# Optimization experiments

Hardware: AMD Instinct MI355X
Metric: run time of the kernel (lower is better)

## Reference

```python
import jax, jax.numpy as jnp
from jax import lax
import numpy as np

IMG = 800
SUB = 16
FS = IMG // SUB            # 50
NA = 9                     # 3 ratios x 3 scales
PRE_NMS = 6000             # test-mode n_test_pre_nms
POST_NMS = 300             # test-mode n_test_post_nms
NMS_THRESH = 0.7
MIN_BOX = 16.0
SLOPE = 0.01               # nn.LeakyReLU default


def build_anchors():
    # Faithful to _generate_anchor: x outer loop, y inner; ctr = grid - 8;
    # anchor rows are [x1, y1, w, h]; ratio outer, scale inner.
    c = np.arange(SUB, (FS + 1) * SUB, SUB).astype(np.float32) - 8.0  # 50 centers
    cx = np.repeat(c, FS)   # x is the outer loop
    cy = np.tile(c, FS)     # y is the inner loop
    rs = np.array([0.5, 1.0, 2.0], dtype=np.float32)
    ss = np.array([8.0, 16.0, 32.0], dtype=np.float32)
    hs = (SUB * ss[None, :] * np.sqrt(rs)[:, None]).reshape(-1)        # [9]
    ws = (SUB * ss[None, :] * np.sqrt(1.0 / rs)[:, None]).reshape(-1)  # [9]
    x1 = cx[:, None] - ws[None, :] / 2.0   # [2500, 9]
    y1 = cy[:, None] - hs[None, :] / 2.0
    w = np.broadcast_to(ws[None, :], x1.shape)
    h = np.broadcast_to(hs[None, :], x1.shape)
    return np.stack([x1, y1, w, h], axis=-1).reshape(-1, 4).astype(np.float32)  # [22500, 4]


def _conv(x, w, b, pad):
    y = lax.conv_general_dilated(x, w, (1, 1), ((pad, pad), (pad, pad)),
                                 dimension_numbers=("NCHW", "OIHW", "NCHW"))
    return y + b[None, :, None, None]


def _nms_keep(boxes):
    # Greedy NMS over score-sorted boxes [P,4] = (x1,y1,x2,y2); returns keep mask.
    x1, y1, x2, y2 = boxes[:, 0], boxes[:, 1], boxes[:, 2], boxes[:, 3]
    area = (x2 - x1 + 1.0) * (y2 - y1 + 1.0)
    P = boxes.shape[0]
    idx = jnp.arange(P)

    def body(i, keep):
        xx1 = jnp.maximum(x1[i], x1)
        yy1 = jnp.maximum(y1[i], y1)
        xx2 = jnp.minimum(x2[i], x2)
        yy2 = jnp.maximum(y2[i], y2)  # faithful to source bug: np.maximum, not minimum
        w = jnp.maximum(0.0, xx2 - xx1 + 1.0)
        h = jnp.maximum(0.0, yy2 - yy1 + 1.0)
        inter = w * h
        ov = inter / (area[i] + area - inter)
        suppress = (ov > NMS_THRESH) & (idx > i) & keep[i]
        return keep & ~suppress

    return lax.fori_loop(0, P, body, jnp.ones((P,), dtype=bool))


def _forward(in_features, conv_w, conv_b, reg_w, reg_b, cls_w, cls_b):
    B = in_features.shape[0]
    feat = _conv(in_features, conv_w, conv_b, 1)
    feat = jnp.where(feat >= 0, feat, SLOPE * feat)  # LeakyReLU(0.01)
    reg = _conv(feat, reg_w, reg_b, 0).transpose(0, 2, 3, 1).reshape(B, -1, 4)
    cls = _conv(feat, cls_w, cls_b, 0).transpose(0, 2, 3, 1).reshape(B, -1, 2)
    cls = jax.nn.softmax(cls, axis=2)

    anchors = jnp.asarray(build_anchors())  # [A,4] = (x1,y1,w,h)
    # The torch loop overwrites `rois` each batch iteration and returns only the
    # last batch's proposals; compute that directly.
    pr = reg[-1]                 # [A,4]
    score = cls[-1, :, 1]        # [A]
    hi = jnp.float32(IMG - 1)
    rx1 = jnp.clip(pr[:, 0] + anchors[:, 0], 0.0, hi)
    ry1 = jnp.clip(pr[:, 1] + anchors[:, 1], 0.0, hi)
    rx2 = jnp.clip(pr[:, 0] + anchors[:, 0] + pr[:, 2] + anchors[:, 2], 0.0, hi)
    ry2 = jnp.clip(pr[:, 1] + anchors[:, 1] + pr[:, 3] + anchors[:, 3], 0.0, hi)
    w = pr[:, 2] + anchors[:, 2]  # unclipped, as in source
    h = pr[:, 3] + anchors[:, 3]
    valid = (w >= MIN_BOX) & (h >= MIN_BOX)
    s = jnp.where(valid, score, -jnp.inf)   # filtered boxes sort to the end
    order = jnp.argsort(-s)[:PRE_NMS]       # top-6000 valid by objectness
    boxes = jnp.stack([rx1, ry1, rx2, ry2], axis=1)[order]  # [PRE,4]

    keep = _nms_keep(lax.stop_gradient(boxes))
    # first POST_NMS surviving boxes, in score order
    sel = jnp.argsort(jnp.where(keep, jnp.arange(PRE_NMS), PRE_NMS))[:POST_NMS]
    kb = boxes[sel]
    # output format: x1, y1, w, h
    return jnp.stack([kb[:, 0], kb[:, 1],
                      kb[:, 2] - kb[:, 0] + 1.0,
                      kb[:, 3] - kb[:, 1] + 1.0], axis=1)


def setup_inputs() -> dict:
    key = jax.random.key(0)
    k = jax.random.split(key, 4)
    return {
        "in_features": jax.random.normal(k[0], (8, 512, FS, FS), dtype=jnp.float32),
        "conv_w": jax.random.normal(k[1], (512, 512, 3, 3), dtype=jnp.float32) * 0.02,
        "conv_b": jnp.zeros((512,), dtype=jnp.float32),
        "reg_w": jax.random.normal(k[2], (36, 512, 1, 1), dtype=jnp.float32) * 0.02,
        "reg_b": jnp.zeros((36,), dtype=jnp.float32),
        "cls_w": jax.random.normal(k[3], (18, 512, 1, 1), dtype=jnp.float32) * 0.02,
        "cls_b": jnp.zeros((18,), dtype=jnp.float32),
    }


def reference(in_features, conv_w, conv_b, reg_w, reg_b, cls_w, cls_b):
    return _forward(in_features, conv_w, conv_b, reg_w, reg_b, cls_w, cls_b)
```

## Files before the change

### kernel.cpp

```cpp
#include <hip/hip_runtime.h>


#define NPIX 2500
#define NANCH 22500
#define NKEY 22528
#define PRE 6000
#define MASKW 94
#define MW 96
#define JCHUNK 1536
#define CS 8
#define KSLOT 8
#define PW 52
#define PSL 2704

__global__ __launch_bounds__(256) void prepK(
    const float* __restrict__ x,
    const float* __restrict__ wt,
    float* __restrict__ xpad,
    float* __restrict__ wtV)
{
    __shared__ float T[64][65];
    const int bx = blockIdx.x;
    if (bx < 512) {
        const int cin = bx;
        const float* src = x + (size_t)cin * NPIX;
        float* dst = xpad + (size_t)cin * PSL;
        for (int i = threadIdx.x; i < PSL; i += 256) {
            const int pr = i / PW;
            const int pc = i - pr * PW;
            float v = 0.f;
            if (pr >= 1 && pr <= 50 && pc >= 1 && pc <= 50)
                v = src[(pr - 1) * 50 + (pc - 1)];
            dst[i] = v;
        }
        return;
    }
    const int idx  = bx - 512;
    const int ct0  = (idx % 72) * 64;
    const int ocb  = (idx / 72) * 64;
    const int tid  = threadIdx.x;
    const int cidx = tid & 63;
    const int r4   = tid >> 6;
    #pragma unroll
    for (int i = 0; i < 16; ++i) {
        const int o = r4 + i * 4;
        T[o][cidx] = wt[(size_t)(ocb + o) * 4608 + ct0 + cidx];
    }
    __syncthreads();
    #pragma unroll
    for (int i = 0; i < 16; ++i) {
        const int ctl = ct0 + r4 + i * 4;
        const int cin = ctl / 9;
        const int t   = ctl - cin * 9;
        const int oc  = ocb + cidx;
        wtV[(((size_t)cin * 64 + (oc >> 3)) * 9 + t) * 8 + (oc & 7)] =
            T[cidx][r4 + i * 4];
    }
}

__global__ __launch_bounds__(256) void conv3x3_v9(
    const float* __restrict__ xpad,
    const float* __restrict__ wtV,
    float* __restrict__ part2)
{
    const int tid  = threadIdx.x;
    const int lane = tid & 63;
    const int wv   = tid >> 6;
    const int ocg  = blockIdx.x;
    const int pb   = blockIdx.y * 4 + wv;
    const int cing = blockIdx.z * 64;
    const int px0  = pb * 64 + lane;
    const int px1  = px0 + 1280;
    const bool act1 = (px1 < NPIX);
    const int r0 = px0 / 50, cc0 = px0 - r0 * 50;
    const int px1c = act1 ? px1 : 0;
    const int r1 = px1c / 50, cc1 = px1c - r1 * 50;

    const float* xb0 = xpad + (size_t)cing * PSL + (r0 + 1) * PW + (cc0 + 1);
    const float* xb1 = xpad + (size_t)cing * PSL + (r1 + 1) * PW + (cc1 + 1);

    float acc0[8], acc1[8];
    #pragma unroll
    for (int j = 0; j < 8; ++j) { acc0[j] = 0.f; acc1[j] = 0.f; }

    const float* wbase = wtV + ((size_t)cing * 64 + ocg) * 72;

    for (int cin = 0; cin < 64; ++cin) {
        float v0[9], v1[9];
        const float* xa = xb0 + (size_t)cin * PSL;
        const float* xc = xb1 + (size_t)cin * PSL;
        #pragma unroll
        for (int t = 0; t < 9; ++t) {
            const int dr = t / 3 - 1, dc = t % 3 - 1;
            v0[t] = xa[dr * PW + dc];
            v1[t] = xc[dr * PW + dc];
        }
        const float* wp = wbase + (size_t)cin * 4608;
        #pragma unroll
        for (int j = 0; j < 8; ++j) {
            float a = acc0[j];
            float b = acc1[j];
            #pragma unroll
            for (int t = 0; t < 9; ++t) {
                const float w = wp[t * 8 + j];
                a = fmaf(w, v0[t], a);
                b = fmaf(w, v1[t], b);
            }
            acc0[j] = a;
            acc1[j] = b;
        }
    }

    float* dst0 = part2 + ((size_t)blockIdx.z * 512 + ocg * 8) * NPIX + px0;
    #pragma unroll
    for (int j = 0; j < 8; ++j)
        dst0[(size_t)j * NPIX] = acc0[j];
    if (act1) {
        float* dst1 = part2 + ((size_t)blockIdx.z * 512 + ocg * 8) * NPIX + px1;
        #pragma unroll
        for (int j = 0; j < 8; ++j)
            dst1[(size_t)j * NPIX] = acc1[j];
    }
}

__global__ __launch_bounds__(256) void reduce_leaky4(
    const float* __restrict__ part2, const float* __restrict__ bias,
    float* __restrict__ feat)
{
    const int oc = blockIdx.x;
    const float b = bias[oc];
    float4* dstv = (float4*)(feat + (size_t)oc * NPIX);
    for (int q = threadIdx.x; q < 625; q += 256) {
        float4 s = make_float4(0.f, 0.f, 0.f, 0.f);
        #pragma unroll
        for (int k = 0; k < CS; ++k) {
            const float4 v = *(const float4*)(part2 + ((size_t)k * 512 + oc) * NPIX + q * 4);
            s.x += v.x; s.y += v.y; s.z += v.z; s.w += v.w;
        }
        s.x += b; s.y += b; s.z += b; s.w += b;
        s.x = (s.x >= 0.f) ? s.x : 0.01f * s.x;
        s.y = (s.y >= 0.f) ? s.y : 0.01f * s.y;
        s.z = (s.z >= 0.f) ? s.z : 0.01f * s.z;
        s.w = (s.w >= 0.f) ? s.w : 0.01f * s.w;
        dstv[q] = s;
    }
}

__global__ __launch_bounds__(256) void conv1x1_heads(
    const float* __restrict__ feat,
    const float* __restrict__ rw, const float* __restrict__ rb,
    const float* __restrict__ cw, const float* __restrict__ cb,
    float* __restrict__ regcls)
{
    __shared__ float sAcc[3][18][64];
    const int tid  = threadIdx.x;
    const int lane = tid & 63;
    const int wv   = tid >> 6;
    const int pix0 = blockIdx.x * 64 + lane;
    const bool act = (pix0 < NPIX);
    const int pix  = act ? pix0 : (NPIX - 1);
    const int chunk = blockIdx.y;
    const float* wb; const float* bb; int ocbase;
    if (chunk == 0)      { wb = rw;            bb = rb;      ocbase = 0;  }
    else if (chunk == 1) { wb = rw + 18 * 512; bb = rb + 18; ocbase = 18; }
    else                 { wb = cw;            bb = cb;      ocbase = 36; }

    float acc[18];
    #pragma unroll
    for (int k = 0; k < 18; ++k) acc[k] = 0.f;

    const int c0 = wv * 128;
    for (int cin = c0; cin < c0 + 128; ++cin) {
        const float v = feat[(size_t)cin * NPIX + pix];
        #pragma unroll
        for (int k = 0; k < 18; ++k)
            acc[k] = fmaf(wb[k * 512 + cin], v, acc[k]);
    }
    if (wv > 0) {
        #pragma unroll
        for (int k = 0; k < 18; ++k) sAcc[wv - 1][k][lane] = acc[k];
    }
    __syncthreads();
    if (wv == 0 && act) {
        #pragma unroll
        for (int k = 0; k < 18; ++k) {
            float s = acc[k];
            s += sAcc[0][k][lane];
            s += sAcc[1][k][lane];
            s += sAcc[2][k][lane];
            regcls[(size_t)(ocbase + k) * NPIX + pix] = s + bb[k];
        }
    }
}

__global__ __launch_bounds__(256) void decodeK(
    const float* __restrict__ regcls,
    float4* __restrict__ boxes,
    unsigned long long* __restrict__ keys)
{
    const int i = blockIdx.x * 256 + threadIdx.x;
    if (i >= NANCH) {
        if (i < NKEY) keys[i] = 0xFFFFFFFFFFFFFFFFull;
        return;
    }
    const int pos = i / 9;
    const int a   = i - pos * 9;
    const int hh  = pos / 50;
    const int wwp = pos - hh * 50;
    const int r = a / 3, s = a - r * 3;

    const float base_s[3] = {128.f, 256.f, 512.f};
    const float sq [3] = {0.70710678118654752440f, 1.0f, 1.41421356237309504880f};
    const float sqi[3] = {1.41421356237309504880f, 1.0f, 0.70710678118654752440f};
    const float hs = base_s[s] * sq[r];
    const float ws = base_s[s] * sqi[r];
    const float cx = (float)(hh * 16 + 8);
    const float cy = (float)(wwp * 16 + 8);
    const float ax = cx - ws * 0.5f;
    const float ay = cy - hs * 0.5f;

    const float pr0 = regcls[(size_t)(a * 4 + 0) * NPIX + pos];
    const float pr1 = regcls[(size_t)(a * 4 + 1) * NPIX + pos];
    const float pr2 = regcls[(size_t)(a * 4 + 2) * NPIX + pos];
    const float pr3 = regcls[(size_t)(a * 4 + 3) * NPIX + pos];
    const float c0  = regcls[(size_t)(36 + a * 2 + 0) * NPIX + pos];
    const float c1  = regcls[(size_t)(36 + a * 2 + 1) * NPIX + pos];

    const float m  = fmaxf(c0, c1);
    const float e0 = expf(c0 - m);
    const float e1 = expf(c1 - m);
    const float score = e1 / (e0 + e1);

    const float t0 = pr0 + ax;
    const float t1 = pr1 + ay;
    const float hi = 799.0f;
    const float rx1 = fminf(fmaxf(t0, 0.f), hi);
    const float ry1 = fminf(fmaxf(t1, 0.f), hi);
    const float rx2 = fminf(fmaxf((t0 + pr2) + ws, 0.f), hi);
    const float ry2 = fminf(fmaxf((t1 + pr3) + hs, 0.f), hi);
    const float bw = pr2 + ws;
    const float bh = pr3 + hs;
    const bool valid = (bw >= 16.f) && (bh >= 16.f);
    const float sc = valid ? score : -__builtin_inff();

    unsigned u = __float_as_uint(sc);
    u = (u & 0x80000000u) ? ~u : (u | 0x80000000u);
    const unsigned k32 = ~u;
    keys[i]  = ((unsigned long long)k32 << 32) | (unsigned)i;
    boxes[i] = make_float4(rx1, ry1, rx2, ry2);
}

__global__ __launch_bounds__(256) void rankK(
    const unsigned long long* __restrict__ keys, int* __restrict__ rank)
{
    const int i = blockIdx.x * 256 + threadIdx.x;
    const unsigned long long my = (i < NANCH) ? keys[i] : 0ull;
    const unsigned long long* kj = keys + blockIdx.y * 2816;
    int cnt = 0;
    for (int t = 0; t < 2816; t += 8) {
        #pragma unroll
        for (int q = 0; q < 8; ++q)
            cnt += (kj[t + q] < my) ? 1 : 0;
    }
    if (i < NANCH) atomicAdd(&rank[i], cnt);
}

__global__ __launch_bounds__(256) void scatterK(
    const float4* __restrict__ boxes, const int* __restrict__ rank,
    float4* __restrict__ sboxes)
{
    const int i = blockIdx.x * 256 + threadIdx.x;
    if (i < NANCH) {
        const int r = rank[i];
        if (r < PRE) sboxes[r] = boxes[i];
    }
}

__global__ __launch_bounds__(256) void nmsMaskK(
    const float4* __restrict__ sb, unsigned long long* __restrict__ mask)
{
    const int tid  = threadIdx.x;
    const int lane = tid & 63;
    const int wv   = tid >> 6;
    const int i0   = blockIdx.x * 16 + wv * 4;
    const int jbase = blockIdx.y * JCHUNK;

    float ix1[4], iy1[4], ix2[4], iy2[4], iar[4];
    #pragma unroll
    for (int ii = 0; ii < 4; ++ii) {
        const float4 b = sb[i0 + ii];
        ix1[ii] = b.x; iy1[ii] = b.y; ix2[ii] = b.z; iy2[ii] = b.w;
        iar[ii] = (b.z - b.x + 1.f) * (b.w - b.y + 1.f);
    }

    for (int w = 0; w < 24; ++w) {
        const int j  = jbase + w * 64 + lane;
        const int jc = (j < PRE) ? j : 0;
        const float4 bj = sb[jc];
        const float jar = (bj.z - bj.x + 1.f) * (bj.w - bj.y + 1.f);
        #pragma unroll
        for (int ii = 0; ii < 4; ++ii) {
            const int i = i0 + ii;
            const float xx1 = fmaxf(ix1[ii], bj.x);
            const float yy1 = fmaxf(iy1[ii], bj.y);
            const float xx2 = fminf(ix2[ii], bj.z);
            const float yy2 = fmaxf(iy2[ii], bj.w);
            const float wvv = fmaxf(0.f, xx2 - xx1 + 1.f);
            const float hvv = fmaxf(0.f, yy2 - yy1 + 1.f);
            const float inter = wvv * hvv;
            const float ov = inter / ((iar[ii] + jar) - inter);
            const bool pred = (j > i) && (j < PRE) && (ov > 0.7f);
            const unsigned long long bits = __ballot(pred);
            if (lane == 0)
                mask[(size_t)i * MW + blockIdx.y * 24 + w] = bits;
        }
    }
}

__global__ __launch_bounds__(64) void nmsScanOutK(
    const unsigned long long* __restrict__ mask,
    const float4* __restrict__ sb,
    float* __restrict__ out)
{
    __shared__ int sKept[300];
    __shared__ unsigned long long sKeepW[MASKW];
    const int lane = threadIdx.x;

    unsigned long long rem0 = 0ull, rem1 = 0ull;
    int cnt = 0;
    int done = 0;

    unsigned long long d00 = mask[(size_t)lane * MW + 0];
    unsigned long long d01 = mask[(size_t)lane * MW + 1];
    unsigned long long d11 = mask[(size_t)(64 + lane) * MW + 1];

    for (int p = 0; p < 47 && !done; ++p) {
        const int g0 = 2 * p, g1 = 2 * p + 1;

        unsigned long long n00 = 0ull, n01 = 0ull, n11 = 0ull;
        if (p + 1 < 47) {
            const int h0 = g0 + 2, h1 = g0 + 3;
            const int ra = h0 * 64 + lane;
            const int rb = h1 * 64 + lane;
            n00 = mask[(size_t)ra * MW + h0];
            n01 = mask[(size_t)ra * MW + h1];
            if (rb < PRE) n11 = mask[(size_t)rb * MW + h1];
        }

        unsigned long long cur0, cur1;
        {
            unsigned lo, hi;
            if (g0 < 64) {
                lo = __builtin_amdgcn_readlane((unsigned)rem0, g0);
                hi = __builtin_amdgcn_readlane((unsigned)(rem0 >> 32), g0);
            } else {
                lo = __builtin_amdgcn_readlane((unsigned)rem1, g0 - 64);
                hi = __builtin_amdgcn_readlane((unsigned)(rem1 >> 32), g0 - 64);
            }
            cur0 = ((unsigned long long)hi << 32) | lo;
            if (g1 < 64) {
                lo = __builtin_amdgcn_readlane((unsigned)rem0, g1);
                hi = __builtin_amdgcn_readlane((unsigned)(rem0 >> 32), g1);
            } else {
                lo = __builtin_amdgcn_readlane((unsigned)rem1, g1 - 64);
                hi = __builtin_amdgcn_readlane((unsigned)(rem1 >> 32), g1 - 64);
            }
            cur1 = ((unsigned long long)hi << 32) | lo;
        }
        const unsigned long long valid0 = ~0ull;
        const unsigned long long valid1 =
            (g1 == MASKW - 1) ? 0x0000FFFFFFFFFFFFull : ~0ull;

        unsigned long long kb0 = 0ull, kb1 = 0ull;
        for (;;) {
            const unsigned long long nd = (~cur0) & valid0;
            if (!nd) break;
            const int b = __builtin_ctzll(nd);
            if (lane == 0 && cnt < 300) sKept[cnt] = g0 * 64 + b;
            ++cnt;
            kb0 |= (1ull << b);
            if (cnt >= 300) { done = 1; break; }
            const unsigned al = __builtin_amdgcn_readlane((unsigned)d00, b);
            const unsigned ah = __builtin_amdgcn_readlane((unsigned)(d00 >> 32), b);
            const unsigned bl = __builtin_amdgcn_readlane((unsigned)d01, b);
            const unsigned bh = __builtin_amdgcn_readlane((unsigned)(d01 >> 32), b);
            cur0 |= (1ull << b) | (((unsigned long long)ah << 32) | al);
            cur1 |= (((unsigned long long)bh << 32) | bl);
        }
        if (!done) {
            for (;;) {
                const unsigned long long nd = (~cur1) & valid1;
                if (!nd) break;
                const int b = __builtin_ctzll(nd);
                if (lane == 0 && cnt < 300) sKept[cnt] = g1 * 64 + b;
                ++cnt;
                kb1 |= (1ull << b);
                if (cnt >= 300) { done = 1; break; }
                const unsigned cl = __builtin_amdgcn_readlane((unsigned)d11, b);
                const unsigned ch = __builtin_amdgcn_readlane((unsigned)(d11 >> 32), b);
                cur1 |= (1ull << b) | (((unsigned long long)ch << 32) | cl);
            }
        }
        if (lane == 0) { sKeepW[g0] = kb0; sKeepW[g1] = kb1; }

        if (!done && (kb0 | kb1)) {
            unsigned long long a0 = 0ull, a1 = 0ull;
            {
                int kbit[KSLOT];
                unsigned long long t = kb0;
                #pragma unroll
                for (int s = 0; s < KSLOT; ++s) {
                    kbit[s] = t ? __builtin_ctzll(t) : 64;
                    t &= t - 1;
                }
                #pragma unroll
                for (int s = 0; s < KSLOT; ++s) {
                    if (kbit[s] < 64) {
                        const unsigned long long* pr =
                            mask + (size_t)(g0 * 64 + kbit[s]) * MW;
                        a0 |= pr[lane];
                        a1 |= (lane < MASKW - 64) ? pr[64 + lane] : 0ull;
                    }
                }
                while (t) {
                    const int b = __builtin_ctzll(t); t &= t - 1;
                    const unsigned long long* pr =
                        mask + (size_t)(g0 * 64 + b) * MW;
                    a0 |= pr[lane];
                    a1 |= (lane < MASKW - 64) ? pr[64 + lane] : 0ull;
                }
            }
            {
                int kbit[KSLOT];
                unsigned long long t = kb1;
                #pragma unroll
                for (int s = 0; s < KSLOT; ++s) {
                    kbit[s] = t ? __builtin_ctzll(t) : 64;
                    t &= t - 1;
                }
                #pragma unroll
                for (int s = 0; s < KSLOT; ++s) {
                    if (kbit[s] < 64) {
                        const unsigned long long* pr =
                            mask + (size_t)(g1 * 64 + kbit[s]) * MW;
                        a0 |= pr[lane];
                        a1 |= (lane < MASKW - 64) ? pr[64 + lane] : 0ull;
                    }
                }
                while (t) {
                    const int b = __builtin_ctzll(t); t &= t - 1;
                    const unsigned long long* pr =
                        mask + (size_t)(g1 * 64 + b) * MW;
                    a0 |= pr[lane];
                    a1 |= (lane < MASKW - 64) ? pr[64 + lane] : 0ull;
                }
            }
            rem0 |= a0;
            rem1 |= a1;
        }
        d00 = n00; d01 = n01; d11 = n11;
    }

    __syncthreads();

    if (cnt < 300) {
        int c = cnt;
        for (int g = 0; g < MASKW && c < 300; ++g) {
            const unsigned long long valid =
                (g == MASKW - 1) ? 0x0000FFFFFFFFFFFFull : ~0ull;
            unsigned long long u = (~sKeepW[g]) & valid;
            while (u && c < 300) {
                const int b = __builtin_ctzll(u); u &= u - 1;
                if (lane == 0) sKept[c] = g * 64 + b;
                ++c;
            }
        }
    }
    __syncthreads();

    for (int s = lane; s < 300; s += 64) {
        const float4 b = sb[sKept[s]];
        out[s * 4 + 0] = b.x;
        out[s * 4 + 1] = b.y;
        out[s * 4 + 2] = b.z - b.x + 1.0f;
        out[s * 4 + 3] = b.w - b.y + 1.0f;
    }
}

extern "C" void kernel_launch(void* const* d_in, const int* in_sizes, int n_in,
                              void* d_out, int out_size, void* d_ws, size_t ws_size,
                              hipStream_t stream)
{
    (void)in_sizes; (void)n_in; (void)out_size; (void)ws_size;
    const float* x   = (const float*)d_in[0] + (size_t)7 * 512 * NPIX;
    const float* cw3 = (const float*)d_in[1];
    const float* cb3 = (const float*)d_in[2];
    const float* rw  = (const float*)d_in[3];
    const float* rb  = (const float*)d_in[4];
    const float* clw = (const float*)d_in[5];
    const float* clb = (const float*)d_in[6];
    float* out = (float*)d_out;

    char* p = (char*)d_ws;
    auto alloc = [&](size_t n) { char* r = p; p += (n + 255) & ~(size_t)255; return r; };
    float*  part2  = (float*)alloc((size_t)CS * 512 * NPIX * 4);
    float*  wtV    = (float*)alloc((size_t)4608 * 512 * 4);
    float*  xpad   = (float*)alloc((size_t)512 * PSL * 4);
    float*  feat   = (float*)alloc((size_t)512 * NPIX * 4);
    float*  regcls = (float*)alloc((size_t)54 * NPIX * 4);
    float4* boxes  = (float4*)alloc((size_t)NANCH * 16);
    unsigned long long* keys = (unsigned long long*)alloc((size_t)NKEY * 8);
    int*    rank   = (int*)alloc((size_t)NANCH * 4);
    float4* sboxes = (float4*)alloc((size_t)PRE * 16);
    unsigned long long* mask = (unsigned long long*)alloc((size_t)PRE * MW * 8);

    hipMemsetAsync(rank, 0, (size_t)NANCH * 4, stream);
    prepK         <<<1088, 256, 0, stream>>>(x, cw3, xpad, wtV);
    conv3x3_v9    <<<dim3(64, 5, CS), 256, 0, stream>>>(xpad, wtV, part2);
    reduce_leaky4 <<<512, 256, 0, stream>>>(part2, cb3, feat);
    conv1x1_heads <<<dim3(40, 3), 256, 0, stream>>>(feat, rw, rb, clw, clb, regcls);
    decodeK       <<<88, 256, 0, stream>>>(regcls, boxes, keys);
    rankK         <<<dim3(88, 8), 256, 0, stream>>>(keys, rank);
    scatterK      <<<88, 256, 0, stream>>>(boxes, rank, sboxes);
    nmsMaskK      <<<dim3(375, 4), 256, 0, stream>>>(sboxes, mask);
    nmsScanOutK   <<<1, 64, 0, stream>>>(mask, sboxes, out);
}
```

Before: 501.7 us.

## Compute three pixels per thread in 3x3 conv, split 1x1 heads, fold rank memset

Each conv3x3 thread now computes three pixels instead of two, so every weight load is reused across more FMAs, and the grid shrinks from 5 to 4 pixel blocks. The 1x1 head kernel is split across a new z dimension of 3, with each block computing 6 output channels instead of 18, which raises parallelism and lowers register use. The rank buffer is now zeroed inside decodeK, which removes a separate memset call. The extra accumulators add register pressure in the conv kernel and may lower occupancy.

Result: faster. 485.1 us (-3.3%).

```diff
diff --git a/kernel.cpp b/kernel.cpp
--- a/kernel.cpp
+++ b/kernel.cpp
@@ -58,7 +58,7 @@
     }
 }
 
-__global__ __launch_bounds__(256) void conv3x3_v9(
+__global__ __launch_bounds__(256) void conv3x3_v13(
     const float* __restrict__ xpad,
     const float* __restrict__ wtV,
     float* __restrict__ part2)
@@ -67,59 +67,69 @@
     const int lane = tid & 63;
     const int wv   = tid >> 6;
     const int ocg  = blockIdx.x;
-    const int pb   = blockIdx.y * 4 + wv;
+    const int wid  = blockIdx.y * 4 + wv;
     const int cing = blockIdx.z * 64;
-    const int px0  = pb * 64 + lane;
-    const int px1  = px0 + 1280;
-    const bool act1 = (px1 < NPIX);
-    const int r0 = px0 / 50, cc0 = px0 - r0 * 50;
-    const int px1c = act1 ? px1 : 0;
-    const int r1 = px1c / 50, cc1 = px1c - r1 * 50;
-
-    const float* xb0 = xpad + (size_t)cing * PSL + (r0 + 1) * PW + (cc0 + 1);
-    const float* xb1 = xpad + (size_t)cing * PSL + (r1 + 1) * PW + (cc1 + 1);
-
-    float acc0[8], acc1[8];
+    const int base = wid * 64 + lane;
+    const int px0  = base;
+    const int px1  = base + 1024;
+    const int px2  = base + 2048;
+    const bool act2 = (px2 < NPIX);
+    const int r0 = px0 / 50, c0 = px0 - r0 * 50;
+    const int r1 = px1 / 50, c1 = px1 - r1 * 50;
+    const int px2c = act2 ? px2 : 0;
+    const int r2 = px2c / 50, c2 = px2c - r2 * 50;
+
+    const float* xb0 = xpad + (size_t)cing * PSL + (r0 + 1) * PW + (c0 + 1);
+    const float* xb1 = xpad + (size_t)cing * PSL + (r1 + 1) * PW + (c1 + 1);
+    const float* xb2 = xpad + (size_t)cing * PSL + (r2 + 1) * PW + (c2 + 1);
+
+    float acc0[8], acc1[8], acc2[8];
     #pragma unroll
-    for (int j = 0; j < 8; ++j) { acc0[j] = 0.f; acc1[j] = 0.f; }
+    for (int j = 0; j < 8; ++j) { acc0[j] = 0.f; acc1[j] = 0.f; acc2[j] = 0.f; }
 
     const float* wbase = wtV + ((size_t)cing * 64 + ocg) * 72;
 
     for (int cin = 0; cin < 64; ++cin) {
-        float v0[9], v1[9];
+        float v0[9], v1[9], v2[9];
         const float* xa = xb0 + (size_t)cin * PSL;
         const float* xc = xb1 + (size_t)cin * PSL;
+        const float* xd = xb2 + (size_t)cin * PSL;
         #pragma unroll
         for (int t = 0; t < 9; ++t) {
             const int dr = t / 3 - 1, dc = t % 3 - 1;
             v0[t] = xa[dr * PW + dc];
             v1[t] = xc[dr * PW + dc];
+            v2[t] = xd[dr * PW + dc];
         }
         const float* wp = wbase + (size_t)cin * 4608;
         #pragma unroll
         for (int j = 0; j < 8; ++j) {
             float a = acc0[j];
             float b = acc1[j];
+            float c = acc2[j];
             #pragma unroll
             for (int t = 0; t < 9; ++t) {
                 const float w = wp[t * 8 + j];
                 a = fmaf(w, v0[t], a);
                 b = fmaf(w, v1[t], b);
+                c = fmaf(w, v2[t], c);
             }
             acc0[j] = a;
             acc1[j] = b;
-        }
-    }
-
-    float* dst0 = part2 + ((size_t)blockIdx.z * 512 + ocg * 8) * NPIX + px0;
+            acc2[j] = c;
+        }
+    }
+
+    float* dst = part2 + ((size_t)blockIdx.z * 512 + ocg * 8) * NPIX;
     #pragma unroll
-    for (int j = 0; j < 8; ++j)
-        dst0[(size_t)j * NPIX] = acc0[j];
-    if (act1) {
-        float* dst1 = part2 + ((size_t)blockIdx.z * 512 + ocg * 8) * NPIX + px1;
+    for (int j = 0; j < 8; ++j) {
+        dst[(size_t)j * NPIX + px0] = acc0[j];
+        dst[(size_t)j * NPIX + px1] = acc1[j];
+    }
+    if (act2) {
         #pragma unroll
         for (int j = 0; j < 8; ++j)
-            dst1[(size_t)j * NPIX] = acc1[j];
+            dst[(size_t)j * NPIX + px2] = acc2[j];
     }
 }
 
@@ -152,7 +162,7 @@
     const float* __restrict__ cw, const float* __restrict__ cb,
     float* __restrict__ regcls)
 {
-    __shared__ float sAcc[3][18][64];
+    __shared__ float sAcc[3][6][64];
     const int tid  = threadIdx.x;
     const int lane = tid & 63;
     const int wv   = tid >> 6;
@@ -160,35 +170,36 @@
     const bool act = (pix0 < NPIX);
     const int pix  = act ? pix0 : (NPIX - 1);
     const int chunk = blockIdx.y;
+    const int k0    = blockIdx.z * 6;
     const float* wb; const float* bb; int ocbase;
     if (chunk == 0)      { wb = rw;            bb = rb;      ocbase = 0;  }
     else if (chunk == 1) { wb = rw + 18 * 512; bb = rb + 18; ocbase = 18; }
     else                 { wb = cw;            bb = cb;      ocbase = 36; }
 
-    float acc[18];
+    float acc[6];
     #pragma unroll
-    for (int k = 0; k < 18; ++k) acc[k] = 0.f;
+    for (int k = 0; k < 6; ++k) acc[k] = 0.f;
 
     const int c0 = wv * 128;
     for (int cin = c0; cin < c0 + 128; ++cin) {
         const float v = feat[(size_t)cin * NPIX + pix];
         #pragma unroll
-        for (int k = 0; k < 18; ++k)
-            acc[k] = fmaf(wb[k * 512 + cin], v, acc[k]);
+        for (int k = 0; k < 6; ++k)
+            acc[k] = fmaf(wb[(k0 + k) * 512 + cin], v, acc[k]);
     }
     if (wv > 0) {
         #pragma unroll
-        for (int k = 0; k < 18; ++k) sAcc[wv - 1][k][lane] = acc[k];
+        for (int k = 0; k < 6; ++k) sAcc[wv - 1][k][lane] = acc[k];
     }
     __syncthreads();
     if (wv == 0 && act) {
         #pragma unroll
-        for (int k = 0; k < 18; ++k) {
+        for (int k = 0; k < 6; ++k) {
             float s = acc[k];
             s += sAcc[0][k][lane];
             s += sAcc[1][k][lane];
             s += sAcc[2][k][lane];
-            regcls[(size_t)(ocbase + k) * NPIX + pix] = s + bb[k];
+            regcls[(size_t)(ocbase + k0 + k) * NPIX + pix] = s + bb[k0 + k];
         }
     }
 }
@@ -196,9 +207,11 @@
 __global__ __launch_bounds__(256) void decodeK(
     const float* __restrict__ regcls,
     float4* __restrict__ boxes,
-    unsigned long long* __restrict__ keys)
+    unsigned long long* __restrict__ keys,
+    int* __restrict__ rank)
 {
     const int i = blockIdx.x * 256 + threadIdx.x;
+    if (i < NANCH) rank[i] = 0;
     if (i >= NANCH) {
         if (i < NKEY) keys[i] = 0xFFFFFFFFFFFFFFFFull;
         return;
@@ -514,12 +527,11 @@
     float4* sboxes = (float4*)alloc((size_t)PRE * 16);
     unsigned long long* mask = (unsigned long long*)alloc((size_t)PRE * MW * 8);
 
-    hipMemsetAsync(rank, 0, (size_t)NANCH * 4, stream);
     prepK         <<<1088, 256, 0, stream>>>(x, cw3, xpad, wtV);
-    conv3x3_v9    <<<dim3(64, 5, CS), 256, 0, stream>>>(xpad, wtV, part2);
+    conv3x3_v13   <<<dim3(64, 4, CS), 256, 0, stream>>>(xpad, wtV, part2);
     reduce_leaky4 <<<512, 256, 0, stream>>>(part2, cb3, feat);
-    conv1x1_heads <<<dim3(40, 3), 256, 0, stream>>>(feat, rw, rb, clw, clb, regcls);
-    decodeK       <<<88, 256, 0, stream>>>(regcls, boxes, keys);
+    conv1x1_heads <<<dim3(40, 3, 3), 256, 0, stream>>>(feat, rw, rb, clw, clb, regcls);
+    decodeK       <<<88, 256, 0, stream>>>(regcls, boxes, keys, rank);
     rankK         <<<dim3(88, 8), 256, 0, stream>>>(keys, rank);
     scatterK      <<<88, 256, 0, stream>>>(boxes, rank, sboxes);
     nmsMaskK      <<<dim3(375, 4), 256, 0, stream>>>(sboxes, mask);
```
